# Kernel optimization log

Hardware: AMD Instinct MI355X
Metric: run time of the kernel (lower is better)

The kernel has to match this reference:

```python
import jax, jax.numpy as jnp
import numpy as np

C = 64   # in_planes
F = 40   # n_freq
T = 512  # n_frame
B = 16


def setup_inputs() -> dict:
    key = jax.random.key(0)
    kx, kq, kk, kv = jax.random.split(key, 4)
    x = jax.random.normal(kx, (B, C, F, T), dtype=jnp.float32)
    # 1x1 conv weights, no bias: [out_ch, in_ch]
    s = 1.0 / np.sqrt(C)
    Wq = jax.random.uniform(kq, (C, C), dtype=jnp.float32, minval=-s, maxval=s)
    Wk = jax.random.uniform(kk, (C, C), dtype=jnp.float32, minval=-s, maxval=s)
    Wv = jax.random.uniform(kv, (C, C), dtype=jnp.float32, minval=-s, maxval=s)
    return {"x": x, "Wq": Wq, "Wk": Wk, "Wv": Wv}


def _proj_tokens(W, x):
    # 1x1 conv (channel mix) then permute(0,3,2,1) + view -> [B, T, F*C]
    y = jnp.einsum('oc,bcft->btfo', W, x)      # [B, T, F, C]
    b, t, f, c = y.shape
    return y.reshape(b, t, f * c)


def reference(x, Wq, Wk, Wv):
    n_batch, n_planes, n_freq, n_frame = x.shape
    d = n_freq * n_planes
    q = _proj_tokens(Wq, x)                     # [B, T, d]
    k = _proj_tokens(Wk, x)
    v = _proj_tokens(Wv, x)
    scores = jnp.einsum('bqd,bkd->bqk', q, k) / jnp.sqrt(jnp.float32(d))
    attn = jax.nn.softmax(scores, axis=-1)      # [B, T, T]
    out = jnp.einsum('bqk,bkd->bqd', attn, v)   # [B, T, d]
    out = out.reshape(n_batch, n_frame, n_freq, n_planes)
    return jnp.transpose(out, (0, 3, 2, 1))     # [B, C, F, T]
```

## Files before the change

kernel.cpp:

```cpp
#include <hip/hip_runtime.h>

constexpr int B_ = 16, C_ = 64, F_ = 40, T_ = 512;
constexpr int D_ = F_ * C_;
constexpr float SCALE = 0.019764235376052372f;

typedef __attribute__((ext_vector_type(8))) short s16x8;
typedef __attribute__((ext_vector_type(4))) short s16x4;
typedef __attribute__((ext_vector_type(4))) float f32x4;

static __device__ __forceinline__ short f2bf(float f) {
  union { float f; unsigned u; } v; v.f = f;
  unsigned r = v.u + 0x7fffu + ((v.u >> 16) & 1u);
  return (short)(r >> 16);
}

static __device__ __forceinline__ f32x4 mfma16(s16x8 a, s16x8 b, f32x4 c) {
  return __builtin_amdgcn_mfma_f32_16x16x32_bf16(a, b, c, 0, 0, 0);
}

static __device__ __forceinline__ void gl2lds16(const short* g, short* l) {
  __builtin_amdgcn_global_load_lds(
      (const __attribute__((address_space(1))) unsigned int*)g,
      (__attribute__((address_space(3))) unsigned int*)l, 16, 0, 0);
}

__global__ __launch_bounds__(256) void wcvt_kernel(
    const float* __restrict__ Wq, const float* __restrict__ Wk,
    const float* __restrict__ Wv, short* __restrict__ Wb,
    float* __restrict__ rowsum)
{
  const int n = blockIdx.x * 256 + threadIdx.x;
  const int p = n >> 9;
  const int r = n & 511;
  const int mi = r >> 7;
  const int ks = (r >> 6) & 1;
  const int lane = r & 63;
  const int o = mi * 16 + (lane & 15);
  const int cb = ks * 32 + (lane >> 4) * 8;
  const float* src = (p == 0) ? Wq : (p == 1) ? Wk : Wv;
  const float sc = (p == 0) ? SCALE : 1.0f;
  const float4 a = *(const float4*)(src + o * 64 + cb);
  const float4 b2 = *(const float4*)(src + o * 64 + cb + 4);
  s16x8 s;
  s[0] = f2bf(a.x * sc);  s[1] = f2bf(a.y * sc);
  s[2] = f2bf(a.z * sc);  s[3] = f2bf(a.w * sc);
  s[4] = f2bf(b2.x * sc); s[5] = f2bf(b2.y * sc);
  s[6] = f2bf(b2.z * sc); s[7] = f2bf(b2.w * sc);
  *(s16x8*)&Wb[n * 8] = s;

  for (int i = n; i < B_ * T_; i += 6 * 256) rowsum[i] = 0.0f;
}

__global__ __launch_bounds__(256, 2) void proj_kernel(
    const float* __restrict__ x, const short* __restrict__ Wb,
    short* __restrict__ Q, short* __restrict__ K, short* __restrict__ V)
{
  constexpr int XS = 132;
  __shared__ __align__(16) short Xl[64 * XS];
  char* Ost = (char*)Xl;

  const int b = blockIdx.z, f = blockIdx.y, tt = blockIdx.x;
  const int tid = threadIdx.x;

  const float* xp = x + (((size_t)b * 64) * 40 + f) * 512 + tt * 128;
  #pragma unroll
  for (int it = 0; it < 8; ++it) {
    const int i = tid + it * 256;
    const int c = i >> 5, j = i & 31;
    const float4 v4 = *(const float4*)(xp + (size_t)c * (F_ * T_) + j * 4);
    s16x4 s4; s4[0] = f2bf(v4.x); s4[1] = f2bf(v4.y);
    s4[2] = f2bf(v4.z); s4[3] = f2bf(v4.w);
    *(s16x4*)&Xl[c * XS + j * 4] = s4;
  }
  __syncthreads();

  const int w = tid >> 6, lane = tid & 63;
  const int quad = lane >> 4, c16 = lane & 15;
  const int tl = w * 32;

  s16x8 bfrag[2][2];
  #pragma unroll
  for (int ni = 0; ni < 2; ++ni)
    #pragma unroll
    for (int ks = 0; ks < 2; ++ks) {
      const int t = tl + ni * 16 + c16;
      const int cb = ks * 32 + quad * 8;
      s16x8 tmp;
      #pragma unroll
      for (int j = 0; j < 8; ++j) tmp[j] = Xl[(cb + j) * XS + t];
      bfrag[ni][ks] = tmp;
    }
  __syncthreads();

  #pragma unroll
  for (int p = 0; p < 3; ++p) {
    s16x8 wfrag[4][2];
    #pragma unroll
    for (int mi = 0; mi < 4; ++mi)
      #pragma unroll
      for (int ks = 0; ks < 2; ++ks)
        wfrag[mi][ks] = *(const s16x8*)(Wb + ((p * 8 + mi * 2 + ks) * 64 + lane) * 8);

    if (p < 2) {
      f32x4 acc[4][2] = {};
      #pragma unroll
      for (int ks = 0; ks < 2; ++ks)
        #pragma unroll
        for (int mi = 0; mi < 4; ++mi)
          #pragma unroll
          for (int ni = 0; ni < 2; ++ni)
            acc[mi][ni] = mfma16(wfrag[mi][ks], bfrag[ni][ks], acc[mi][ni]);
      __syncthreads();
      #pragma unroll
      for (int mi = 0; mi < 4; ++mi)
        #pragma unroll
        for (int ni = 0; ni < 2; ++ni) {
          const int trow = tl + ni * 16 + c16;
          unsigned addr = trow * 128 + (mi * 32 + quad * 8);
          addr ^= (unsigned)((trow & 7) << 4);
          s16x4 s4;
          #pragma unroll
          for (int r = 0; r < 4; ++r) s4[r] = f2bf(acc[mi][ni][r]);
          *(s16x4*)(Ost + addr) = s4;
        }
      __syncthreads();
      short* outp = (p == 0) ? Q : K;
      #pragma unroll
      for (int pass = 0; pass < 4; ++pass) {
        const int row = pass * 32 + (tid >> 3);
        const int s16off = tid & 7;
        unsigned a2 = row * 128 + s16off * 16;
        a2 ^= (unsigned)((row & 7) << 4);
        const s16x8 vz = *(const s16x8*)(Ost + a2);
        *(s16x8*)&outp[(size_t)(b * 512 + tt * 128 + row) * D_ + f * 64 + s16off * 8] = vz;
      }
    } else {
      f32x4 acc[2][4] = {};
      #pragma unroll
      for (int ks = 0; ks < 2; ++ks)
        #pragma unroll
        for (int ni = 0; ni < 2; ++ni)
          #pragma unroll
          for (int mi = 0; mi < 4; ++mi)
            acc[ni][mi] = mfma16(bfrag[ni][ks], wfrag[mi][ks], acc[ni][mi]);
      __syncthreads();
      #pragma unroll
      for (int ni = 0; ni < 2; ++ni)
        #pragma unroll
        for (int mi = 0; mi < 4; ++mi) {
          const int orow = mi * 16 + c16;
          unsigned addr = orow * 256 + (tl + ni * 16 + quad * 4) * 2;
          addr ^= (unsigned)((orow & 7) << 4);
          s16x4 s4;
          #pragma unroll
          for (int r = 0; r < 4; ++r) s4[r] = f2bf(acc[ni][mi][r]);
          *(s16x4*)(Ost + addr) = s4;
        }
      __syncthreads();
      #pragma unroll
      for (int pass = 0; pass < 4; ++pass) {
        const int row = pass * 16 + (tid >> 4);
        const int s16off = tid & 15;
        unsigned a2 = row * 256 + s16off * 16;
        a2 ^= (unsigned)((row & 7) << 4);
        const s16x8 vz = *(const s16x8*)(Ost + a2);
        *(s16x8*)&V[((size_t)(b * D_ + f * 64 + row)) * 512 + tt * 128 + s16off * 8] = vz;
      }
    }
    if (p < 2) __syncthreads();
  }
}

__global__ __launch_bounds__(256) void scores_kernel(
    const short* __restrict__ Q, const short* __restrict__ K,
    short* __restrict__ A, float* __restrict__ rowsum)
{
  __shared__ __align__(16) short As[64 * 64];
  __shared__ __align__(16) short Bs[128 * 64];
  const int b = blockIdx.y;
  const int mt = blockIdx.x >> 2, nt = blockIdx.x & 3;
  const int m0 = mt * 64, n0 = nt * 128;
  const int tid = threadIdx.x;
  const int w = tid >> 6, lane = tid & 63, quad = lane >> 4, c16 = lane & 15;
  const int wm = (w >> 1) * 32, wn = (w & 1) * 64;

  const short* qb = Q + (size_t)(b * 512 + m0) * D_;
  const short* kb = K + (size_t)(b * 512 + n0) * D_;

  const short* agp[2];
  short* aldsb[2];
  #pragma unroll
  for (int i = 0; i < 2; ++i) {
    const int s = i * 256 + tid, row = s >> 3;
    const int g = (s & 7) ^ (row & 7);
    agp[i] = qb + (size_t)row * D_ + g * 8;
    aldsb[i] = &As[(i * 256 + w * 64) * 8];
  }
  const short* bgp[4];
  short* bldsb[4];
  #pragma unroll
  for (int i = 0; i < 4; ++i) {
    const int s = i * 256 + tid, row = s >> 3;
    const int g = (s & 7) ^ (row & 7);
    bgp[i] = kb + (size_t)row * D_ + g * 8;
    bldsb[i] = &Bs[(i * 256 + w * 64) * 8];
  }

  const short* amp[2][2];
  #pragma unroll
  for (int mi = 0; mi < 2; ++mi)
    #pragma unroll
    for (int ks = 0; ks < 2; ++ks) {
      const int row = wm + mi * 16 + c16;
      const int g = (ks * 4 + quad) ^ (row & 7);
      amp[mi][ks] = &As[row * 64 + g * 8];
    }
  const short* bmp[4][2];
  #pragma unroll
  for (int ni = 0; ni < 4; ++ni)
    #pragma unroll
    for (int ks = 0; ks < 2; ++ks) {
      const int row = wn + ni * 16 + c16;
      const int g = (ks * 4 + quad) ^ (row & 7);
      bmp[ni][ks] = &Bs[row * 64 + g * 8];
    }

  f32x4 acc[2][4] = {};
  constexpr int NK = D_ / 64;
  for (int kk = 0; kk < NK; ++kk) {
    const int ko = kk * 64;
    __syncthreads();
    #pragma unroll
    for (int i = 0; i < 2; ++i) gl2lds16(agp[i] + ko, aldsb[i]);
    #pragma unroll
    for (int i = 0; i < 4; ++i) gl2lds16(bgp[i] + ko, bldsb[i]);
    __syncthreads();
    s16x8 am[2][2], bm[4][2];
    #pragma unroll
    for (int mi = 0; mi < 2; ++mi)
      #pragma unroll
      for (int ks = 0; ks < 2; ++ks) am[mi][ks] = *(const s16x8*)amp[mi][ks];
    #pragma unroll
    for (int ni = 0; ni < 4; ++ni)
      #pragma unroll
      for (int ks = 0; ks < 2; ++ks) bm[ni][ks] = *(const s16x8*)bmp[ni][ks];
    #pragma unroll
    for (int ks = 0; ks < 2; ++ks)
      #pragma unroll
      for (int mi = 0; mi < 2; ++mi)
        #pragma unroll
        for (int ni = 0; ni < 4; ++ni)
          acc[mi][ni] = mfma16(am[mi][ks], bm[ni][ks], acc[mi][ni]);
  }

  float* rsb = rowsum + b * 512;
  #pragma unroll
  for (int mi = 0; mi < 2; ++mi)
    #pragma unroll
    for (int r = 0; r < 4; ++r) {
      float part = 0.f;
      #pragma unroll
      for (int ni = 0; ni < 4; ++ni) {
        const float e0 = __expf(acc[mi][ni][r]);
        acc[mi][ni][r] = e0;
        part += e0;
      }
      #pragma unroll
      for (int mask = 1; mask < 16; mask <<= 1) part += __shfl_xor(part, mask);
      if (c16 == 0)
        atomicAdd(&rsb[m0 + wm + mi * 16 + quad * 4 + r], part);
    }

  short* ap = A + ((size_t)b * 512) * 512;
  #pragma unroll
  for (int mi = 0; mi < 2; ++mi)
    #pragma unroll
    for (int ni = 0; ni < 4; ++ni) {
      const int kcol = n0 + wn + ni * 16 + c16;
      const int qr = m0 + wm + mi * 16 + quad * 4;
      #pragma unroll
      for (int r = 0; r < 4; ++r)
        ap[(size_t)(qr + r) * 512 + kcol] = f2bf(acc[mi][ni][r]);
    }
}

__global__ __launch_bounds__(256) void pv_kernel(
    const short* __restrict__ A, const short* __restrict__ V,
    const float* __restrict__ rowsum, float* __restrict__ out)
{
  __shared__ __align__(16) short As[128 * 64];
  __shared__ __align__(16) short Bs[128 * 64];
  const int b = blockIdx.y;
  const int mt = blockIdx.x / 20, dt = blockIdx.x % 20;
  const int m0 = mt * 128, n0 = dt * 128;
  const int tid = threadIdx.x;
  const int w = tid >> 6, lane = tid & 63, quad = lane >> 4, c16 = lane & 15;
  const int wm = (w >> 1) * 64, wn = (w & 1) * 64;

  const short* ab = A + ((size_t)b * 512 + m0) * 512;
  const short* vb = V + ((size_t)b * D_ + n0) * 512;

  const short* agp[4]; short* aldsb[4];
  const short* bgp[4]; short* bldsb[4];
  #pragma unroll
  for (int i = 0; i < 4; ++i) {
    const int s = i * 256 + tid, row = s >> 3;
    const int g = (s & 7) ^ (row & 7);
    agp[i] = ab + (size_t)row * 512 + g * 8;
    bgp[i] = vb + (size_t)row * 512 + g * 8;
    aldsb[i] = &As[(i * 256 + w * 64) * 8];
    bldsb[i] = &Bs[(i * 256 + w * 64) * 8];
  }

  const short* amp[4][2];
  const short* bmp[4][2];
  #pragma unroll
  for (int mi = 0; mi < 4; ++mi)
    #pragma unroll
    for (int ks = 0; ks < 2; ++ks) {
      const int rowa = wm + mi * 16 + c16;
      const int rowb = wn + mi * 16 + c16;
      amp[mi][ks] = &As[rowa * 64 + (((ks * 4 + quad) ^ (rowa & 7)) * 8)];
      bmp[mi][ks] = &Bs[rowb * 64 + (((ks * 4 + quad) ^ (rowb & 7)) * 8)];
    }

  f32x4 acc[4][4] = {};
  constexpr int NK = 512 / 64;
  for (int kk = 0; kk < NK; ++kk) {
    const int ko = kk * 64;
    __syncthreads();
    #pragma unroll
    for (int i = 0; i < 4; ++i) gl2lds16(agp[i] + ko, aldsb[i]);
    #pragma unroll
    for (int i = 0; i < 4; ++i) gl2lds16(bgp[i] + ko, bldsb[i]);
    __syncthreads();
    s16x8 am[4][2], bm[4][2];
    #pragma unroll
    for (int mi = 0; mi < 4; ++mi)
      #pragma unroll
      for (int ks = 0; ks < 2; ++ks) {
        am[mi][ks] = *(const s16x8*)amp[mi][ks];
        bm[mi][ks] = *(const s16x8*)bmp[mi][ks];
      }
    #pragma unroll
    for (int ks = 0; ks < 2; ++ks)
      #pragma unroll
      for (int mi = 0; mi < 4; ++mi)
        #pragma unroll
        for (int ni = 0; ni < 4; ++ni)
          acc[mi][ni] = mfma16(am[mi][ks], bm[ni][ks], acc[mi][ni]);
  }

  const float* rsb = rowsum + b * 512;
  #pragma unroll
  for (int mi = 0; mi < 4; ++mi) {
    const int t = m0 + wm + mi * 16 + quad * 4;
    const float4 rs = *(const float4*)(rsb + t);
    const float i0 = 1.0f / rs.x, i1 = 1.0f / rs.y;
    const float i2 = 1.0f / rs.z, i3 = 1.0f / rs.w;
    #pragma unroll
    for (int ni = 0; ni < 4; ++ni) {
      acc[mi][ni][0] *= i0; acc[mi][ni][1] *= i1;
      acc[mi][ni][2] *= i2; acc[mi][ni][3] *= i3;
    }
  }

  #pragma unroll
  for (int mi = 0; mi < 4; ++mi)
    #pragma unroll
    for (int ni = 0; ni < 4; ++ni) {
      const int d = n0 + wn + ni * 16 + c16;
      const int ff = d >> 6, cc = d & 63;
      const int t = m0 + wm + mi * 16 + quad * 4;
      float4 o4;
      o4.x = acc[mi][ni][0]; o4.y = acc[mi][ni][1];
      o4.z = acc[mi][ni][2]; o4.w = acc[mi][ni][3];
      *(float4*)&out[(((size_t)b * 64 + cc) * 40 + ff) * 512 + t] = o4;
    }
}

extern "C" void kernel_launch(void* const* d_in, const int* in_sizes, int n_in,
                              void* d_out, int out_size, void* d_ws, size_t ws_size,
                              hipStream_t stream)
{
  const float* x  = (const float*)d_in[0];
  const float* Wq = (const float*)d_in[1];
  const float* Wk = (const float*)d_in[2];
  const float* Wv = (const float*)d_in[3];
  float* out = (float*)d_out;

  char* ws = (char*)d_ws;
  constexpr size_t QB = (size_t)B_ * T_ * D_ * 2;
  constexpr size_t AB = (size_t)B_ * T_ * T_ * 2;
  short* Q  = (short*)(ws);
  short* Kt = (short*)(ws + QB);
  short* Vt = (short*)(ws + 2 * QB);
  short* At = (short*)(ws + 3 * QB);
  short* Wb = (short*)(ws + 3 * QB + AB);
  float* rowsum = (float*)(ws + 3 * QB + AB + 24576);

  wcvt_kernel<<<dim3(6), 256, 0, stream>>>(Wq, Wk, Wv, Wb, rowsum);
  proj_kernel<<<dim3(4, 40, 16), 256, 0, stream>>>(x, Wb, Q, Kt, Vt);
  scores_kernel<<<dim3(32, 16), 256, 0, stream>>>(Q, Kt, At, rowsum);
  pv_kernel<<<dim3(80, 16), 256, 0, stream>>>(At, Vt, rowsum, out);
}
```

Baseline: 248.3 us.

## Double-buffer LDS tiles in scores and PV GEMM kernels

Doubles the shared-memory tiles in both the scores and PV kernels and issues the asynchronous global-to-LDS loads for the next K slice before computing on the current one. The goal is to overlap memory traffic with MFMA work and to go from two barriers per K step to one. In exchange, LDS use per block doubles, which can lower occupancy. The async loads now rely on the single trailing barrier, with no explicit vmcnt wait, to be complete before they are read.

After: 255.6 us. 2.9% more time.

```diff
diff --git a/kernel.cpp b/kernel.cpp
--- a/kernel.cpp
+++ b/kernel.cpp
@@ -175,8 +175,10 @@
     const short* __restrict__ Q, const short* __restrict__ K,
     short* __restrict__ A, float* __restrict__ rowsum)
 {
-  __shared__ __align__(16) short As[64 * 64];
-  __shared__ __align__(16) short Bs[128 * 64];
+  constexpr int AOFF = 64 * 64;
+  constexpr int BOFF = 128 * 64;
+  __shared__ __align__(16) short As[2 * 64 * 64];
+  __shared__ __align__(16) short Bs[2 * 128 * 64];
   const int b = blockIdx.y;
   const int mt = blockIdx.x >> 2, nt = blockIdx.x & 3;
   const int m0 = mt * 64, n0 = nt * 128;
@@ -225,32 +227,68 @@
       bmp[ni][ks] = &Bs[row * 64 + g * 8];
     }
 
+  #pragma unroll
+  for (int i = 0; i < 2; ++i) gl2lds16(agp[i], aldsb[i]);
+  #pragma unroll
+  for (int i = 0; i < 4; ++i) gl2lds16(bgp[i], bldsb[i]);
+  __syncthreads();
+
   f32x4 acc[2][4] = {};
   constexpr int NK = D_ / 64;
-  for (int kk = 0; kk < NK; ++kk) {
-    const int ko = kk * 64;
-    __syncthreads();
-    #pragma unroll
-    for (int i = 0; i < 2; ++i) gl2lds16(agp[i] + ko, aldsb[i]);
-    #pragma unroll
-    for (int i = 0; i < 4; ++i) gl2lds16(bgp[i] + ko, bldsb[i]);
-    __syncthreads();
-    s16x8 am[2][2], bm[4][2];
-    #pragma unroll
-    for (int mi = 0; mi < 2; ++mi)
-      #pragma unroll
-      for (int ks = 0; ks < 2; ++ks) am[mi][ks] = *(const s16x8*)amp[mi][ks];
-    #pragma unroll
-    for (int ni = 0; ni < 4; ++ni)
-      #pragma unroll
-      for (int ks = 0; ks < 2; ++ks) bm[ni][ks] = *(const s16x8*)bmp[ni][ks];
-    #pragma unroll
-    for (int ks = 0; ks < 2; ++ks)
+  #pragma unroll 1
+  for (int kk = 0; kk < NK; kk += 2) {
+    {
+      const int ko = (kk + 1) * 64;
+      #pragma unroll
+      for (int i = 0; i < 2; ++i) gl2lds16(agp[i] + ko, aldsb[i] + AOFF);
+      #pragma unroll
+      for (int i = 0; i < 4; ++i) gl2lds16(bgp[i] + ko, bldsb[i] + BOFF);
+      s16x8 am[2][2], bm[4][2];
       #pragma unroll
       for (int mi = 0; mi < 2; ++mi)
         #pragma unroll
-        for (int ni = 0; ni < 4; ++ni)
-          acc[mi][ni] = mfma16(am[mi][ks], bm[ni][ks], acc[mi][ni]);
+        for (int ks = 0; ks < 2; ++ks) am[mi][ks] = *(const s16x8*)amp[mi][ks];
+      #pragma unroll
+      for (int ni = 0; ni < 4; ++ni)
+        #pragma unroll
+        for (int ks = 0; ks < 2; ++ks) bm[ni][ks] = *(const s16x8*)bmp[ni][ks];
+      #pragma unroll
+      for (int ks = 0; ks < 2; ++ks)
+        #pragma unroll
+        for (int mi = 0; mi < 2; ++mi)
+          #pragma unroll
+          for (int ni = 0; ni < 4; ++ni)
+            acc[mi][ni] = mfma16(am[mi][ks], bm[ni][ks], acc[mi][ni]);
+      __syncthreads();
+    }
+    {
+      if (kk + 2 < NK) {
+        const int ko = (kk + 2) * 64;
+        #pragma unroll
+        for (int i = 0; i < 2; ++i) gl2lds16(agp[i] + ko, aldsb[i]);
+        #pragma unroll
+        for (int i = 0; i < 4; ++i) gl2lds16(bgp[i] + ko, bldsb[i]);
+      }
+      s16x8 am[2][2], bm[4][2];
+      #pragma unroll
+      for (int mi = 0; mi < 2; ++mi)
+        #pragma unroll
+        for (int ks = 0; ks < 2; ++ks)
+          am[mi][ks] = *(const s16x8*)(amp[mi][ks] + AOFF);
+      #pragma unroll
+      for (int ni = 0; ni < 4; ++ni)
+        #pragma unroll
+        for (int ks = 0; ks < 2; ++ks)
+          bm[ni][ks] = *(const s16x8*)(bmp[ni][ks] + BOFF);
+      #pragma unroll
+      for (int ks = 0; ks < 2; ++ks)
+        #pragma unroll
+        for (int mi = 0; mi < 2; ++mi)
+          #pragma unroll
+          for (int ni = 0; ni < 4; ++ni)
+            acc[mi][ni] = mfma16(am[mi][ks], bm[ni][ks], acc[mi][ni]);
+      __syncthreads();
+    }
   }
 
   float* rsb = rowsum + b * 512;
@@ -288,8 +326,9 @@
     const short* __restrict__ A, const short* __restrict__ V,
     const float* __restrict__ rowsum, float* __restrict__ out)
 {
-  __shared__ __align__(16) short As[128 * 64];
-  __shared__ __align__(16) short Bs[128 * 64];
+  constexpr int AOFF = 128 * 64;
+  __shared__ __align__(16) short As[2 * 128 * 64];
+  __shared__ __align__(16) short Bs[2 * 128 * 64];
   const int b = blockIdx.y;
   const int mt = blockIdx.x / 20, dt = blockIdx.x % 20;
   const int m0 = mt * 128, n0 = dt * 128;
@@ -324,31 +363,64 @@
       bmp[mi][ks] = &Bs[rowb * 64 + (((ks * 4 + quad) ^ (rowb & 7)) * 8)];
     }
 
+  #pragma unroll
+  for (int i = 0; i < 4; ++i) gl2lds16(agp[i], aldsb[i]);
+  #pragma unroll
+  for (int i = 0; i < 4; ++i) gl2lds16(bgp[i], bldsb[i]);
+  __syncthreads();
+
   f32x4 acc[4][4] = {};
   constexpr int NK = 512 / 64;
-  for (int kk = 0; kk < NK; ++kk) {
-    const int ko = kk * 64;
-    __syncthreads();
-    #pragma unroll
-    for (int i = 0; i < 4; ++i) gl2lds16(agp[i] + ko, aldsb[i]);
-    #pragma unroll
-    for (int i = 0; i < 4; ++i) gl2lds16(bgp[i] + ko, bldsb[i]);
-    __syncthreads();
-    s16x8 am[4][2], bm[4][2];
-    #pragma unroll
-    for (int mi = 0; mi < 4; ++mi)
-      #pragma unroll
-      for (int ks = 0; ks < 2; ++ks) {
-        am[mi][ks] = *(const s16x8*)amp[mi][ks];
-        bm[mi][ks] = *(const s16x8*)bmp[mi][ks];
+  #pragma unroll 1
+  for (int kk = 0; kk < NK; kk += 2) {
+    {
+      const int ko = (kk + 1) * 64;
+      #pragma unroll
+      for (int i = 0; i < 4; ++i) gl2lds16(agp[i] + ko, aldsb[i] + AOFF);
+      #pragma unroll
+      for (int i = 0; i < 4; ++i) gl2lds16(bgp[i] + ko, bldsb[i] + AOFF);
+      s16x8 am[4][2], bm[4][2];
+      #pragma unroll
+      for (int mi = 0; mi < 4; ++mi)
+        #pragma unroll
+        for (int ks = 0; ks < 2; ++ks) {
+          am[mi][ks] = *(const s16x8*)amp[mi][ks];
+          bm[mi][ks] = *(const s16x8*)bmp[mi][ks];
+        }
+      #pragma unroll
+      for (int ks = 0; ks < 2; ++ks)
+        #pragma unroll
+        for (int mi = 0; mi < 4; ++mi)
+          #pragma unroll
+          for (int ni = 0; ni < 4; ++ni)
+            acc[mi][ni] = mfma16(am[mi][ks], bm[ni][ks], acc[mi][ni]);
+      __syncthreads();
+    }
+    {
+      if (kk + 2 < NK) {
+        const int ko = (kk + 2) * 64;
+        #pragma unroll
+        for (int i = 0; i < 4; ++i) gl2lds16(agp[i] + ko, aldsb[i]);
+        #pragma unroll
+        for (int i = 0; i < 4; ++i) gl2lds16(bgp[i] + ko, bldsb[i]);
       }
-    #pragma unroll
-    for (int ks = 0; ks < 2; ++ks)
+      s16x8 am[4][2], bm[4][2];
       #pragma unroll
       for (int mi = 0; mi < 4; ++mi)
         #pragma unroll
-        for (int ni = 0; ni < 4; ++ni)
-          acc[mi][ni] = mfma16(am[mi][ks], bm[ni][ks], acc[mi][ni]);
+        for (int ks = 0; ks < 2; ++ks) {
+          am[mi][ks] = *(const s16x8*)(amp[mi][ks] + AOFF);
+          bm[mi][ks] = *(const s16x8*)(bmp[mi][ks] + AOFF);
+        }
+      #pragma unroll
+      for (int ks = 0; ks < 2; ++ks)
+        #pragma unroll
+        for (int mi = 0; mi < 4; ++mi)
+          #pragma unroll
+          for (int ni = 0; ni < 4; ++ni)
+            acc[mi][ni] = mfma16(am[mi][ks], bm[ni][ks], acc[mi][ni]);
+      __syncthreads();
+    }
   }
 
   const float* rsb = rowsum + b * 512;
```

## Double-buffer scores GEMM with larger tiles and interleave batches in grid order

Applied to the files above, without the earlier changes.

The scores kernel moves from 64x128 to 128x128 tiles and double-buffers its LDS K-slices, so the global-to-LDS loads for the next slice overlap the MFMA work on the current one, and it needs only one barrier per step. Both the scores and PV kernels now use a flattened 1D grid with the batch index in the low bits, which changes the order blocks are scheduled and their L2 locality. The bigger tiles halve the scores grid to 256 blocks, which is about one wave on a 256-CU part, and double the LDS use and register pressure per block.

New measurement: 258.3 us. +4.1%, slower.

```diff
diff --git a/kernel.cpp b/kernel.cpp
--- a/kernel.cpp
+++ b/kernel.cpp
@@ -175,87 +175,108 @@
     const short* __restrict__ Q, const short* __restrict__ K,
     short* __restrict__ A, float* __restrict__ rowsum)
 {
-  __shared__ __align__(16) short As[64 * 64];
-  __shared__ __align__(16) short Bs[128 * 64];
-  const int b = blockIdx.y;
-  const int mt = blockIdx.x >> 2, nt = blockIdx.x & 3;
-  const int m0 = mt * 64, n0 = nt * 128;
+  constexpr int OFF = 128 * 64;
+  __shared__ __align__(16) short As[2 * 128 * 64];
+  __shared__ __align__(16) short Bs[2 * 128 * 64];
+  const int xid = blockIdx.x;
+  const int b = xid & 15;
+  const int tile = xid >> 4;
+  const int mt = tile >> 2, nt = tile & 3;
+  const int m0 = mt * 128, n0 = nt * 128;
   const int tid = threadIdx.x;
   const int w = tid >> 6, lane = tid & 63, quad = lane >> 4, c16 = lane & 15;
-  const int wm = (w >> 1) * 32, wn = (w & 1) * 64;
+  const int wm = (w >> 1) * 64, wn = (w & 1) * 64;
 
   const short* qb = Q + (size_t)(b * 512 + m0) * D_;
   const short* kb = K + (size_t)(b * 512 + n0) * D_;
 
-  const short* agp[2];
-  short* aldsb[2];
-  #pragma unroll
-  for (int i = 0; i < 2; ++i) {
+  const short* agp[4]; short* aldsb[4];
+  const short* bgp[4]; short* bldsb[4];
+  #pragma unroll
+  for (int i = 0; i < 4; ++i) {
     const int s = i * 256 + tid, row = s >> 3;
     const int g = (s & 7) ^ (row & 7);
     agp[i] = qb + (size_t)row * D_ + g * 8;
+    bgp[i] = kb + (size_t)row * D_ + g * 8;
     aldsb[i] = &As[(i * 256 + w * 64) * 8];
-  }
-  const short* bgp[4];
-  short* bldsb[4];
-  #pragma unroll
-  for (int i = 0; i < 4; ++i) {
-    const int s = i * 256 + tid, row = s >> 3;
-    const int g = (s & 7) ^ (row & 7);
-    bgp[i] = kb + (size_t)row * D_ + g * 8;
     bldsb[i] = &Bs[(i * 256 + w * 64) * 8];
   }
 
-  const short* amp[2][2];
-  #pragma unroll
-  for (int mi = 0; mi < 2; ++mi)
+  const short* amp[4][2];
+  const short* bmp[4][2];
+  #pragma unroll
+  for (int mi = 0; mi < 4; ++mi)
     #pragma unroll
     for (int ks = 0; ks < 2; ++ks) {
-      const int row = wm + mi * 16 + c16;
-      const int g = (ks * 4 + quad) ^ (row & 7);
-      amp[mi][ks] = &As[row * 64 + g * 8];
-    }
-  const short* bmp[4][2];
-  #pragma unroll
-  for (int ni = 0; ni < 4; ++ni)
-    #pragma unroll
-    for (int ks = 0; ks < 2; ++ks) {
-      const int row = wn + ni * 16 + c16;
-      const int g = (ks * 4 + quad) ^ (row & 7);
-      bmp[ni][ks] = &Bs[row * 64 + g * 8];
-    }
-
-  f32x4 acc[2][4] = {};
+      const int rowa = wm + mi * 16 + c16;
+      const int rowb = wn + mi * 16 + c16;
+      amp[mi][ks] = &As[rowa * 64 + (((ks * 4 + quad) ^ (rowa & 7)) * 8)];
+      bmp[mi][ks] = &Bs[rowb * 64 + (((ks * 4 + quad) ^ (rowb & 7)) * 8)];
+    }
+
+  #pragma unroll
+  for (int i = 0; i < 4; ++i) gl2lds16(agp[i], aldsb[i]);
+  #pragma unroll
+  for (int i = 0; i < 4; ++i) gl2lds16(bgp[i], bldsb[i]);
+  __syncthreads();
+
+  f32x4 acc[4][4] = {};
   constexpr int NK = D_ / 64;
-  for (int kk = 0; kk < NK; ++kk) {
-    const int ko = kk * 64;
-    __syncthreads();
-    #pragma unroll
-    for (int i = 0; i < 2; ++i) gl2lds16(agp[i] + ko, aldsb[i]);
-    #pragma unroll
-    for (int i = 0; i < 4; ++i) gl2lds16(bgp[i] + ko, bldsb[i]);
-    __syncthreads();
-    s16x8 am[2][2], bm[4][2];
-    #pragma unroll
-    for (int mi = 0; mi < 2; ++mi)
-      #pragma unroll
-      for (int ks = 0; ks < 2; ++ks) am[mi][ks] = *(const s16x8*)amp[mi][ks];
-    #pragma unroll
-    for (int ni = 0; ni < 4; ++ni)
-      #pragma unroll
-      for (int ks = 0; ks < 2; ++ks) bm[ni][ks] = *(const s16x8*)bmp[ni][ks];
-    #pragma unroll
-    for (int ks = 0; ks < 2; ++ks)
-      #pragma unroll
-      for (int mi = 0; mi < 2; ++mi)
-        #pragma unroll
-        for (int ni = 0; ni < 4; ++ni)
-          acc[mi][ni] = mfma16(am[mi][ks], bm[ni][ks], acc[mi][ni]);
+  #pragma unroll 1
+  for (int kk = 0; kk < NK; kk += 2) {
+    {
+      const int ko = (kk + 1) * 64;
+      #pragma unroll
+      for (int i = 0; i < 4; ++i) gl2lds16(agp[i] + ko, aldsb[i] + OFF);
+      #pragma unroll
+      for (int i = 0; i < 4; ++i) gl2lds16(bgp[i] + ko, bldsb[i] + OFF);
+      s16x8 am[4][2], bm[4][2];
+      #pragma unroll
+      for (int mi = 0; mi < 4; ++mi)
+        #pragma unroll
+        for (int ks = 0; ks < 2; ++ks) {
+          am[mi][ks] = *(const s16x8*)amp[mi][ks];
+          bm[mi][ks] = *(const s16x8*)bmp[mi][ks];
+        }
+      #pragma unroll
+      for (int ks = 0; ks < 2; ++ks)
+        #pragma unroll
+        for (int mi = 0; mi < 4; ++mi)
+          #pragma unroll
+          for (int ni = 0; ni < 4; ++ni)
+            acc[mi][ni] = mfma16(am[mi][ks], bm[ni][ks], acc[mi][ni]);
+      __syncthreads();
+    }
+    {
+      if (kk + 2 < NK) {
+        const int ko = (kk + 2) * 64;
+        #pragma unroll
+        for (int i = 0; i < 4; ++i) gl2lds16(agp[i] + ko, aldsb[i]);
+        #pragma unroll
+        for (int i = 0; i < 4; ++i) gl2lds16(bgp[i] + ko, bldsb[i]);
+      }
+      s16x8 am[4][2], bm[4][2];
+      #pragma unroll
+      for (int mi = 0; mi < 4; ++mi)
+        #pragma unroll
+        for (int ks = 0; ks < 2; ++ks) {
+          am[mi][ks] = *(const s16x8*)(amp[mi][ks] + OFF);
+          bm[mi][ks] = *(const s16x8*)(bmp[mi][ks] + OFF);
+        }
+      #pragma unroll
+      for (int ks = 0; ks < 2; ++ks)
+        #pragma unroll
+        for (int mi = 0; mi < 4; ++mi)
+          #pragma unroll
+          for (int ni = 0; ni < 4; ++ni)
+            acc[mi][ni] = mfma16(am[mi][ks], bm[ni][ks], acc[mi][ni]);
+      __syncthreads();
+    }
   }
 
   float* rsb = rowsum + b * 512;
   #pragma unroll
-  for (int mi = 0; mi < 2; ++mi)
+  for (int mi = 0; mi < 4; ++mi)
     #pragma unroll
     for (int r = 0; r < 4; ++r) {
       float part = 0.f;
@@ -273,7 +294,7 @@
 
   short* ap = A + ((size_t)b * 512) * 512;
   #pragma unroll
-  for (int mi = 0; mi < 2; ++mi)
+  for (int mi = 0; mi < 4; ++mi)
     #pragma unroll
     for (int ni = 0; ni < 4; ++ni) {
       const int kcol = n0 + wn + ni * 16 + c16;
@@ -290,8 +311,10 @@
 {
   __shared__ __align__(16) short As[128 * 64];
   __shared__ __align__(16) short Bs[128 * 64];
-  const int b = blockIdx.y;
-  const int mt = blockIdx.x / 20, dt = blockIdx.x % 20;
+  const int xid = blockIdx.x;
+  const int b = xid & 15;
+  const int tile = xid >> 4;
+  const int mt = tile / 20, dt = tile % 20;
   const int m0 = mt * 128, n0 = dt * 128;
   const int tid = threadIdx.x;
   const int w = tid >> 6, lane = tid & 63, quad = lane >> 4, c16 = lane & 15;
@@ -401,6 +424,6 @@
 
   wcvt_kernel<<<dim3(6), 256, 0, stream>>>(Wq, Wk, Wv, Wb, rowsum);
   proj_kernel<<<dim3(4, 40, 16), 256, 0, stream>>>(x, Wb, Q, Kt, Vt);
-  scores_kernel<<<dim3(32, 16), 256, 0, stream>>>(Q, Kt, At, rowsum);
-  pv_kernel<<<dim3(80, 16), 256, 0, stream>>>(At, Vt, rowsum, out);
-}
+  scores_kernel<<<dim3(256), 256, 0, stream>>>(Q, Kt, At, rowsum);
+  pv_kernel<<<dim3(1280), 256, 0, stream>>>(At, Vt, rowsum, out);
+}
```

## Fold Wq and Wk into one Gram matrix and drop Q/K projections

Applied to the files above, without the earlier changes.

Precomputes G = Wq^T·Wk (scaled) in a prep kernel. The projection kernel now writes only a bf16 copy of x in token layout plus V, instead of separate Q and K tensors. The scores kernel multiplies each Q-side x tile by G on the fly before the QK^T MFMA and reads raw x for the K side. This removes one full projection and one large intermediate tensor's write and read traffic. In exchange it adds a small GEMM and an extra LDS round-trip with a sync in every k-step of the scores loop, and it rounds G·x to bf16, which changes numerics.

Result: slower. 264.4 us (+6.5%).

```diff
diff --git a/kernel.cpp b/kernel.cpp
--- a/kernel.cpp
+++ b/kernel.cpp
@@ -24,36 +24,58 @@
       (__attribute__((address_space(3))) unsigned int*)l, 16, 0, 0);
 }
 
-__global__ __launch_bounds__(256) void wcvt_kernel(
+__global__ __launch_bounds__(256) void prep_kernel(
     const float* __restrict__ Wq, const float* __restrict__ Wk,
     const float* __restrict__ Wv, short* __restrict__ Wb,
-    float* __restrict__ rowsum)
+    short* __restrict__ Gt, float* __restrict__ rowsum)
 {
-  const int n = blockIdx.x * 256 + threadIdx.x;
-  const int p = n >> 9;
-  const int r = n & 511;
-  const int mi = r >> 7;
-  const int ks = (r >> 6) & 1;
-  const int lane = r & 63;
-  const int o = mi * 16 + (lane & 15);
-  const int cb = ks * 32 + (lane >> 4) * 8;
-  const float* src = (p == 0) ? Wq : (p == 1) ? Wk : Wv;
-  const float sc = (p == 0) ? SCALE : 1.0f;
-  const float4 a = *(const float4*)(src + o * 64 + cb);
-  const float4 b2 = *(const float4*)(src + o * 64 + cb + 4);
-  s16x8 s;
-  s[0] = f2bf(a.x * sc);  s[1] = f2bf(a.y * sc);
-  s[2] = f2bf(a.z * sc);  s[3] = f2bf(a.w * sc);
-  s[4] = f2bf(b2.x * sc); s[5] = f2bf(b2.y * sc);
-  s[6] = f2bf(b2.z * sc); s[7] = f2bf(b2.w * sc);
-  *(s16x8*)&Wb[n * 8] = s;
-
-  for (int i = n; i < B_ * T_; i += 6 * 256) rowsum[i] = 0.0f;
+  __shared__ float lq[4096], lk[4096];
+  const int blk = blockIdx.x, tid = threadIdx.x;
+  if (blk < 2) {
+    const int n = blk * 256 + tid;
+    const int mi = n >> 7, ks = (n >> 6) & 1, lane = n & 63;
+    const int o = mi * 16 + (lane & 15);
+    const int cb = ks * 32 + (lane >> 4) * 8;
+    const float4 a = *(const float4*)(Wv + o * 64 + cb);
+    const float4 b2 = *(const float4*)(Wv + o * 64 + cb + 4);
+    s16x8 s;
+    s[0] = f2bf(a.x);  s[1] = f2bf(a.y);
+    s[2] = f2bf(a.z);  s[3] = f2bf(a.w);
+    s[4] = f2bf(b2.x); s[5] = f2bf(b2.y);
+    s[6] = f2bf(b2.z); s[7] = f2bf(b2.w);
+    *(s16x8*)&Wb[n * 8] = s;
+  } else {
+    for (int i = tid; i < 1024; i += 256) {
+      *(float4*)&lq[i * 4] = *(const float4*)(Wq + i * 4);
+      *(float4*)&lk[i * 4] = *(const float4*)(Wk + i * 4);
+    }
+    __syncthreads();
+    #pragma unroll
+    for (int gi = 0; gi < 2; ++gi) {
+      const int g = gi * 256 + tid;
+      const int mi = g >> 7, ks = (g >> 6) & 1, lane = g & 63;
+      const int cm = mi * 16 + (lane & 15);
+      const int cb = ks * 32 + (lane >> 4) * 8;
+      float s[8] = {};
+      for (int o = 0; o < 64; ++o) {
+        const float ko = lk[o * 64 + cm];
+        const float4 a0 = *(const float4*)&lq[o * 64 + cb];
+        const float4 a1 = *(const float4*)&lq[o * 64 + cb + 4];
+        s[0] += a0.x * ko; s[1] += a0.y * ko; s[2] += a0.z * ko; s[3] += a0.w * ko;
+        s[4] += a1.x * ko; s[5] += a1.y * ko; s[6] += a1.z * ko; s[7] += a1.w * ko;
+      }
+      s16x8 sv;
+      #pragma unroll
+      for (int j = 0; j < 8; ++j) sv[j] = f2bf(s[j] * SCALE);
+      *(s16x8*)&Gt[g * 8] = sv;
+    }
+    for (int i = tid; i < B_ * T_; i += 256) rowsum[i] = 0.0f;
+  }
 }
 
 __global__ __launch_bounds__(256, 2) void proj_kernel(
     const float* __restrict__ x, const short* __restrict__ Wb,
-    short* __restrict__ Q, short* __restrict__ K, short* __restrict__ V)
+    short* __restrict__ Xb, short* __restrict__ V)
 {
   constexpr int XS = 132;
   __shared__ __align__(16) short Xl[64 * XS];
@@ -93,90 +115,72 @@
   __syncthreads();
 
   #pragma unroll
-  for (int p = 0; p < 3; ++p) {
-    s16x8 wfrag[4][2];
-    #pragma unroll
-    for (int mi = 0; mi < 4; ++mi)
-      #pragma unroll
-      for (int ks = 0; ks < 2; ++ks)
-        wfrag[mi][ks] = *(const s16x8*)(Wb + ((p * 8 + mi * 2 + ks) * 64 + lane) * 8);
-
-    if (p < 2) {
-      f32x4 acc[4][2] = {};
-      #pragma unroll
-      for (int ks = 0; ks < 2; ++ks)
-        #pragma unroll
-        for (int mi = 0; mi < 4; ++mi)
-          #pragma unroll
-          for (int ni = 0; ni < 2; ++ni)
-            acc[mi][ni] = mfma16(wfrag[mi][ks], bfrag[ni][ks], acc[mi][ni]);
-      __syncthreads();
+  for (int ni = 0; ni < 2; ++ni)
+    #pragma unroll
+    for (int ks = 0; ks < 2; ++ks) {
+      const int trow = tl + ni * 16 + c16;
+      unsigned addr = trow * 128 + ks * 64 + quad * 16;
+      addr ^= (unsigned)((trow & 7) << 4);
+      *(s16x8*)(Ost + addr) = bfrag[ni][ks];
+    }
+  __syncthreads();
+  #pragma unroll
+  for (int pass = 0; pass < 4; ++pass) {
+    const int row = pass * 32 + (tid >> 3);
+    const int s16off = tid & 7;
+    unsigned a2 = row * 128 + s16off * 16;
+    a2 ^= (unsigned)((row & 7) << 4);
+    const s16x8 vz = *(const s16x8*)(Ost + a2);
+    *(s16x8*)&Xb[(size_t)(b * 512 + tt * 128 + row) * D_ + f * 64 + s16off * 8] = vz;
+  }
+  __syncthreads();
+
+  s16x8 wfrag[4][2];
+  #pragma unroll
+  for (int mi = 0; mi < 4; ++mi)
+    #pragma unroll
+    for (int ks = 0; ks < 2; ++ks)
+      wfrag[mi][ks] = *(const s16x8*)(Wb + ((mi * 2 + ks) * 64 + lane) * 8);
+
+  f32x4 acc[2][4] = {};
+  #pragma unroll
+  for (int ks = 0; ks < 2; ++ks)
+    #pragma unroll
+    for (int ni = 0; ni < 2; ++ni)
       #pragma unroll
       for (int mi = 0; mi < 4; ++mi)
-        #pragma unroll
-        for (int ni = 0; ni < 2; ++ni) {
-          const int trow = tl + ni * 16 + c16;
-          unsigned addr = trow * 128 + (mi * 32 + quad * 8);
-          addr ^= (unsigned)((trow & 7) << 4);
-          s16x4 s4;
-          #pragma unroll
-          for (int r = 0; r < 4; ++r) s4[r] = f2bf(acc[mi][ni][r]);
-          *(s16x4*)(Ost + addr) = s4;
-        }
-      __syncthreads();
-      short* outp = (p == 0) ? Q : K;
-      #pragma unroll
-      for (int pass = 0; pass < 4; ++pass) {
-        const int row = pass * 32 + (tid >> 3);
-        const int s16off = tid & 7;
-        unsigned a2 = row * 128 + s16off * 16;
-        a2 ^= (unsigned)((row & 7) << 4);
-        const s16x8 vz = *(const s16x8*)(Ost + a2);
-        *(s16x8*)&outp[(size_t)(b * 512 + tt * 128 + row) * D_ + f * 64 + s16off * 8] = vz;
-      }
-    } else {
-      f32x4 acc[2][4] = {};
-      #pragma unroll
-      for (int ks = 0; ks < 2; ++ks)
-        #pragma unroll
-        for (int ni = 0; ni < 2; ++ni)
-          #pragma unroll
-          for (int mi = 0; mi < 4; ++mi)
-            acc[ni][mi] = mfma16(bfrag[ni][ks], wfrag[mi][ks], acc[ni][mi]);
-      __syncthreads();
-      #pragma unroll
-      for (int ni = 0; ni < 2; ++ni)
-        #pragma unroll
-        for (int mi = 0; mi < 4; ++mi) {
-          const int orow = mi * 16 + c16;
-          unsigned addr = orow * 256 + (tl + ni * 16 + quad * 4) * 2;
-          addr ^= (unsigned)((orow & 7) << 4);
-          s16x4 s4;
-          #pragma unroll
-          for (int r = 0; r < 4; ++r) s4[r] = f2bf(acc[ni][mi][r]);
-          *(s16x4*)(Ost + addr) = s4;
-        }
-      __syncthreads();
-      #pragma unroll
-      for (int pass = 0; pass < 4; ++pass) {
-        const int row = pass * 16 + (tid >> 4);
-        const int s16off = tid & 15;
-        unsigned a2 = row * 256 + s16off * 16;
-        a2 ^= (unsigned)((row & 7) << 4);
-        const s16x8 vz = *(const s16x8*)(Ost + a2);
-        *(s16x8*)&V[((size_t)(b * D_ + f * 64 + row)) * 512 + tt * 128 + s16off * 8] = vz;
-      }
-    }
-    if (p < 2) __syncthreads();
+        acc[ni][mi] = mfma16(bfrag[ni][ks], wfrag[mi][ks], acc[ni][mi]);
+  #pragma unroll
+  for (int ni = 0; ni < 2; ++ni)
+    #pragma unroll
+    for (int mi = 0; mi < 4; ++mi) {
+      const int orow = mi * 16 + c16;
+      unsigned addr = orow * 256 + (tl + ni * 16 + quad * 4) * 2;
+      addr ^= (unsigned)((orow & 7) << 4);
+      s16x4 s4;
+      #pragma unroll
+      for (int r = 0; r < 4; ++r) s4[r] = f2bf(acc[ni][mi][r]);
+      *(s16x4*)(Ost + addr) = s4;
+    }
+  __syncthreads();
+  #pragma unroll
+  for (int pass = 0; pass < 4; ++pass) {
+    const int row = pass * 16 + (tid >> 4);
+    const int s16off = tid & 15;
+    unsigned a2 = row * 256 + s16off * 16;
+    a2 ^= (unsigned)((row & 7) << 4);
+    const s16x8 vz = *(const s16x8*)(Ost + a2);
+    *(s16x8*)&V[((size_t)(b * D_ + f * 64 + row)) * 512 + tt * 128 + s16off * 8] = vz;
   }
 }
 
 __global__ __launch_bounds__(256) void scores_kernel(
-    const short* __restrict__ Q, const short* __restrict__ K,
+    const short* __restrict__ Xb, const short* __restrict__ Gt,
     short* __restrict__ A, float* __restrict__ rowsum)
 {
   __shared__ __align__(16) short As[64 * 64];
   __shared__ __align__(16) short Bs[128 * 64];
+  __shared__ __align__(16) short YA[64 * 64];
   const int b = blockIdx.y;
   const int mt = blockIdx.x >> 2, nt = blockIdx.x & 3;
   const int m0 = mt * 64, n0 = nt * 128;
@@ -184,11 +188,17 @@
   const int w = tid >> 6, lane = tid & 63, quad = lane >> 4, c16 = lane & 15;
   const int wm = (w >> 1) * 32, wn = (w & 1) * 64;
 
-  const short* qb = Q + (size_t)(b * 512 + m0) * D_;
-  const short* kb = K + (size_t)(b * 512 + n0) * D_;
-
-  const short* agp[2];
-  short* aldsb[2];
+  const short* qb = Xb + (size_t)(b * 512 + m0) * D_;
+  const short* kb = Xb + (size_t)(b * 512 + n0) * D_;
+
+  s16x8 gt[4][2];
+  #pragma unroll
+  for (int mi = 0; mi < 4; ++mi)
+    #pragma unroll
+    for (int ks = 0; ks < 2; ++ks)
+      gt[mi][ks] = *(const s16x8*)(Gt + ((mi * 2 + ks) * 64 + lane) * 8);
+
+  const short* agp[2]; short* aldsb[2];
   #pragma unroll
   for (int i = 0; i < 2; ++i) {
     const int s = i * 256 + tid, row = s >> 3;
@@ -196,8 +206,7 @@
     agp[i] = qb + (size_t)row * D_ + g * 8;
     aldsb[i] = &As[(i * 256 + w * 64) * 8];
   }
-  const short* bgp[4];
-  short* bldsb[4];
+  const short* bgp[4]; short* bldsb[4];
   #pragma unroll
   for (int i = 0; i < 4; ++i) {
     const int s = i * 256 + tid, row = s >> 3;
@@ -206,6 +215,23 @@
     bldsb[i] = &Bs[(i * 256 + w * 64) * 8];
   }
 
+  const short* xrp[2];
+  #pragma unroll
+  for (int ks = 0; ks < 2; ++ks) {
+    const int row = w * 16 + c16;
+    const int g = (ks * 4 + quad) ^ (row & 7);
+    xrp[ks] = &As[row * 64 + g * 8];
+  }
+  char* ywp[4];
+  {
+    const int t1 = w * 16 + c16;
+    #pragma unroll
+    for (int mi = 0; mi < 4; ++mi) {
+      unsigned addr = t1 * 128 + mi * 32 + quad * 8;
+      addr ^= (unsigned)((t1 & 7) << 4);
+      ywp[mi] = (char*)YA + addr;
+    }
+  }
   const short* amp[2][2];
   #pragma unroll
   for (int mi = 0; mi < 2; ++mi)
@@ -213,7 +239,7 @@
     for (int ks = 0; ks < 2; ++ks) {
       const int row = wm + mi * 16 + c16;
       const int g = (ks * 4 + quad) ^ (row & 7);
-      amp[mi][ks] = &As[row * 64 + g * 8];
+      amp[mi][ks] = &YA[row * 64 + g * 8];
     }
   const short* bmp[4][2];
   #pragma unroll
@@ -235,15 +261,33 @@
     #pragma unroll
     for (int i = 0; i < 4; ++i) gl2lds16(bgp[i] + ko, bldsb[i]);
     __syncthreads();
-    s16x8 am[2][2], bm[4][2];
+    s16x8 bm[4][2];
+    #pragma unroll
+    for (int ni = 0; ni < 4; ++ni)
+      #pragma unroll
+      for (int ks = 0; ks < 2; ++ks) bm[ni][ks] = *(const s16x8*)bmp[ni][ks];
+    s16x8 xbf[2];
+    #pragma unroll
+    for (int ks = 0; ks < 2; ++ks) xbf[ks] = *(const s16x8*)xrp[ks];
+    f32x4 y[4] = {};
+    #pragma unroll
+    for (int ks = 0; ks < 2; ++ks)
+      #pragma unroll
+      for (int mi = 0; mi < 4; ++mi)
+        y[mi] = mfma16(gt[mi][ks], xbf[ks], y[mi]);
+    #pragma unroll
+    for (int mi = 0; mi < 4; ++mi) {
+      s16x4 s4;
+      #pragma unroll
+      for (int r = 0; r < 4; ++r) s4[r] = f2bf(y[mi][r]);
+      *(s16x4*)ywp[mi] = s4;
+    }
+    __syncthreads();
+    s16x8 am[2][2];
     #pragma unroll
     for (int mi = 0; mi < 2; ++mi)
       #pragma unroll
       for (int ks = 0; ks < 2; ++ks) am[mi][ks] = *(const s16x8*)amp[mi][ks];
-    #pragma unroll
-    for (int ni = 0; ni < 4; ++ni)
-      #pragma unroll
-      for (int ks = 0; ks < 2; ++ks) bm[ni][ks] = *(const s16x8*)bmp[ni][ks];
     #pragma unroll
     for (int ks = 0; ks < 2; ++ks)
       #pragma unroll
@@ -392,15 +436,15 @@
   char* ws = (char*)d_ws;
   constexpr size_t QB = (size_t)B_ * T_ * D_ * 2;
   constexpr size_t AB = (size_t)B_ * T_ * T_ * 2;
-  short* Q  = (short*)(ws);
-  short* Kt = (short*)(ws + QB);
-  short* Vt = (short*)(ws + 2 * QB);
-  short* At = (short*)(ws + 3 * QB);
-  short* Wb = (short*)(ws + 3 * QB + AB);
-  float* rowsum = (float*)(ws + 3 * QB + AB + 24576);
-
-  wcvt_kernel<<<dim3(6), 256, 0, stream>>>(Wq, Wk, Wv, Wb, rowsum);
-  proj_kernel<<<dim3(4, 40, 16), 256, 0, stream>>>(x, Wb, Q, Kt, Vt);
-  scores_kernel<<<dim3(32, 16), 256, 0, stream>>>(Q, Kt, At, rowsum);
+  short* Xb = (short*)(ws);
+  short* Vt = (short*)(ws + QB);
+  short* At = (short*)(ws + 2 * QB);
+  short* Wb = (short*)(ws + 2 * QB + AB);
+  short* Gt = (short*)(ws + 2 * QB + AB + 8192);
+  float* rowsum = (float*)(ws + 2 * QB + AB + 16384);
+
+  prep_kernel<<<dim3(3), 256, 0, stream>>>(Wq, Wk, Wv, Wb, Gt, rowsum);
+  proj_kernel<<<dim3(4, 40, 16), 256, 0, stream>>>(x, Wb, Xb, Vt);
+  scores_kernel<<<dim3(32, 16), 256, 0, stream>>>(Xb, Gt, At, rowsum);
   pv_kernel<<<dim3(80, 16), 256, 0, stream>>>(At, Vt, rowsum, out);
 }
```
